# Kernel optimization log

Hardware: AMD Instinct MI355X
Metric: run time of the kernel (lower is better)

Reference implementation:

```python
import jax, jax.numpy as jnp
import numpy as np

N = 100000
NNZ = 3200000
F = 128


def setup_inputs() -> dict:
    key = jax.random.key(0)
    k1, k2, k3 = jax.random.split(key, 3)
    x = jax.random.normal(k1, (N, F), dtype=jnp.float32)
    A_ind = jax.random.randint(k2, (2, NNZ), 0, N, dtype=jnp.int64)
    A_val = jax.random.normal(k3, (NNZ,), dtype=jnp.float32)
    return {"x": x, "A_ind": A_ind, "A_val": A_val}


def reference(x, A_ind, A_val):
    # COO SpMM: out[r] = sum over edges e with row[e]==r of A_val[e] * x[col[e]]
    # coalesce() in torch sums duplicate (row, col) entries; segment_sum over
    # rows yields identical math without explicit sorting/deduplication.
    row, col = A_ind[0], A_ind[1]
    contrib = A_val[:, None] * x[col]            # [nnz, F] gather + scale
    out = jax.ops.segment_sum(contrib, row, num_segments=x.shape[0])  # scatter-add
    return out
```

## Files before the change

### kernel.cpp

```cpp
#include <hip/hip_runtime.h>

#define F 128
#define RPB 64
#define MAXNB 1792
#define CHUNK 8192
#define EPT 32
#define CAP 3072
#define SPMM_T 512
#define HELD (CAP/SPMM_T)
#define PERSIST 1024

__global__ void spmm_coo_atomic(const int* __restrict__ rows,
                                const int* __restrict__ cols,
                                const float* __restrict__ vals,
                                const float* __restrict__ x,
                                float* __restrict__ out,
                                int nnz, int n_rows) {
    int t = blockIdx.x * blockDim.x + threadIdx.x;
    int e = t >> 5;
    int g = t & 31;
    if (e >= nnz) return;
    int r = rows[e];
    int c = cols[e];
    float v = vals[e];
    if ((unsigned)r >= (unsigned)n_rows || (unsigned)c >= (unsigned)n_rows) return;
    const float4 xv = *reinterpret_cast<const float4*>(x + (size_t)c * F + g * 4);
    float* o = out + (size_t)r * F + g * 4;
    atomicAdd(o + 0, v * xv.x);
    atomicAdd(o + 1, v * xv.y);
    atomicAdd(o + 2, v * xv.z);
    atomicAdd(o + 3, v * xv.w);
}

__device__ __forceinline__ unsigned f2bf(float f) {
    unsigned u = __float_as_uint(f);
    return (u + 0x7FFFu + ((u >> 16) & 1u)) >> 16;
}

__global__ void k_cvt_histo(const float* __restrict__ x, unsigned short* __restrict__ xb,
                            long long xtotal,
                            const int* __restrict__ rows, int* __restrict__ cnt,
                            int nnz, int nbk, int n, int cvtb) {
    __shared__ int lc[MAXNB];
    if ((int)blockIdx.x < cvtb) {
        long long i = ((long long)blockIdx.x * 256 + threadIdx.x) * 8;
        if (i >= xtotal) return;
        float4 a = *reinterpret_cast<const float4*>(x + i);
        float4 b = *reinterpret_cast<const float4*>(x + i + 4);
        uint4 o;
        o.x = f2bf(a.x) | (f2bf(a.y) << 16);
        o.y = f2bf(a.z) | (f2bf(a.w) << 16);
        o.z = f2bf(b.x) | (f2bf(b.y) << 16);
        o.w = f2bf(b.z) | (f2bf(b.w) << 16);
        *reinterpret_cast<uint4*>(xb + i) = o;
    } else {
        for (int i = threadIdx.x; i < nbk; i += 256) lc[i] = 0;
        __syncthreads();
        int base = ((int)blockIdx.x - cvtb) * CHUNK;
#pragma unroll
        for (int k = 0; k < EPT; ++k) {
            int e = base + k * 256 + threadIdx.x;
            if (e < nnz) {
                int r = rows[e];
                if ((unsigned)r < (unsigned)n) atomicAdd(&lc[r / RPB], 1);
            }
        }
        __syncthreads();
        for (int i = threadIdx.x; i < nbk; i += 256) {
            int c = lc[i];
            if (c) atomicAdd(&cnt[i], c);
        }
    }
}

__global__ void k_bucket_scan(const int* __restrict__ cnt, int* __restrict__ off,
                              int* __restrict__ gcur, int nbk) {
    __shared__ int s[256];
    int tid = threadIdx.x;
    int per = (nbk + 255) / 256;
    int base = tid * per;
    int loc[8];
    int tsum = 0;
#pragma unroll
    for (int k = 0; k < 8; ++k) {
        int i = base + k;
        int v = (k < per && i < nbk) ? cnt[i] : 0;
        loc[k] = v;
        tsum += v;
    }
    s[tid] = tsum;
    __syncthreads();
    for (int o = 1; o < 256; o <<= 1) {
        int t = (tid >= o) ? s[tid - o] : 0;
        __syncthreads();
        s[tid] += t;
        __syncthreads();
    }
    int run = s[tid] - tsum;
#pragma unroll
    for (int k = 0; k < 8; ++k) {
        int i = base + k;
        if (k < per && i < nbk) { off[i] = run; gcur[i] = run; }
        run += loc[k];
    }
    if (tid == 255) off[nbk] = s[255];
}

__global__ void k_rank_scatter(const int* __restrict__ rows, const int* __restrict__ cols,
                               const float* __restrict__ vals, int* __restrict__ gcur,
                               int2* __restrict__ pair, int nnz, int nbk, int n) {
    __shared__ int lcnt[MAXNB];
    __shared__ int lbase[MAXNB];
    for (int i = threadIdx.x; i < nbk; i += 256) lcnt[i] = 0;
    __syncthreads();
    int base = blockIdx.x * CHUNK;
    unsigned br[EPT];
#pragma unroll
    for (int k = 0; k < EPT; ++k) {
        int e = base + k * 256 + threadIdx.x;
        br[k] = 0xFFFFFFFFu;
        if (e < nnz) {
            int r = rows[e];
            if ((unsigned)r < (unsigned)n) {
                int b = r / RPB;
                int rk = atomicAdd(&lcnt[b], 1);
                br[k] = ((unsigned)b << 13) | (unsigned)rk;
            }
        }
    }
    __syncthreads();
    for (int i = threadIdx.x; i < nbk; i += 256) {
        int c = lcnt[i];
        if (c) lbase[i] = atomicAdd(&gcur[i], c);
    }
    __syncthreads();
#pragma unroll
    for (int k = 0; k < EPT; ++k) {
        if (br[k] != 0xFFFFFFFFu) {
            int e = base + k * 256 + threadIdx.x;
            int b = br[k] >> 13;
            int rk = br[k] & 0x1FFF;
            int lr = rows[e] - b * RPB;
            int c = cols[e];
            if ((unsigned)c >= (unsigned)n) c = 0;
            int pos = lbase[b] + rk;
            pair[pos] = make_int2((lr << 17) | c, __float_as_int(vals[e]));
        }
    }
}

__global__ void __launch_bounds__(SPMM_T) k_sort_spmm(const int* __restrict__ off,
                                                      const int2* __restrict__ pair,
                                                      const unsigned short* __restrict__ xb,
                                                      float* __restrict__ out,
                                                      int n, int nbk) {
    __shared__ int2 eb[CAP];
    __shared__ int rcnt[RPB];
    __shared__ int rst[RPB + 1];
    __shared__ int rcur[RPB];

    int tid = threadIdx.x;
    int wave = tid >> 6;
    int lane = tid & 63;
    int q = lane >> 4;
    int fl = lane & 15;

    for (int b = blockIdx.x; b < nbk; b += gridDim.x) {
        int beg = off[b], end = off[b + 1];
        bool first = true;
        int bb = beg;
        do {
            int bn = min(CAP, end - bb);
            if (tid < RPB) rcnt[tid] = 0;
            __syncthreads();

            int2 held[HELD];
#pragma unroll
            for (int k = 0; k < HELD; ++k) {
                int j = tid + k * SPMM_T;
                held[k] = make_int2(0, 0);
                if (j < bn) {
                    int2 pr = pair[bb + j];
                    held[k] = pr;
                    atomicAdd(&rcnt[pr.x >> 17], 1);
                }
            }
            __syncthreads();

            if (tid < RPB) {
                int v = rcnt[tid];
                int s = v;
                for (int o = 1; o < RPB; o <<= 1) {
                    int t = __shfl_up(s, o);
                    if (tid >= o) s += t;
                }
                rst[tid + 1] = s;
                if (tid == 0) rst[0] = 0;
                rcur[tid] = s - v;
            }
            __syncthreads();

#pragma unroll
            for (int k = 0; k < HELD; ++k) {
                int j = tid + k * SPMM_T;
                if (j < bn) {
                    int2 pr = held[k];
                    int lr = pr.x >> 17;
                    int pos = atomicAdd(&rcur[lr], 1);
                    eb[pos] = make_int2(pr.x & 0x1FFFF, pr.y);
                }
            }
            __syncthreads();

            for (int rr = 0; rr < 8; ++rr) {
                int lr = wave * 8 + rr;
                int s0 = rst[lr], s1 = rst[lr + 1];
                float acc[8] = {0.f, 0.f, 0.f, 0.f, 0.f, 0.f, 0.f, 0.f};
#pragma unroll 2
                for (int j = s0 + q; j < s1; j += 4) {
                    int2 e = eb[j];
                    int col = e.x;
                    float vk = __int_as_float(e.y);
                    uint4 w = *reinterpret_cast<const uint4*>(xb + (size_t)col * F + fl * 8);
                    acc[0] += vk * __uint_as_float(w.x << 16);
                    acc[1] += vk * __uint_as_float(w.x & 0xFFFF0000u);
                    acc[2] += vk * __uint_as_float(w.y << 16);
                    acc[3] += vk * __uint_as_float(w.y & 0xFFFF0000u);
                    acc[4] += vk * __uint_as_float(w.z << 16);
                    acc[5] += vk * __uint_as_float(w.z & 0xFFFF0000u);
                    acc[6] += vk * __uint_as_float(w.w << 16);
                    acc[7] += vk * __uint_as_float(w.w & 0xFFFF0000u);
                }
#pragma unroll
                for (int i = 0; i < 8; ++i) {
                    acc[i] += __shfl_xor(acc[i], 16);
                    acc[i] += __shfl_xor(acc[i], 32);
                }
                if (q == 0) {
                    long long row = (long long)b * RPB + lr;
                    if (row < n) {
                        float* po = out + (size_t)row * F + fl * 8;
                        float4 lo = make_float4(acc[0], acc[1], acc[2], acc[3]);
                        float4 hi = make_float4(acc[4], acc[5], acc[6], acc[7]);
                        if (first) {
                            *reinterpret_cast<float4*>(po) = lo;
                            *reinterpret_cast<float4*>(po + 4) = hi;
                        } else {
                            float4 t0 = *reinterpret_cast<const float4*>(po);
                            float4 t1 = *reinterpret_cast<const float4*>(po + 4);
                            t0.x += lo.x; t0.y += lo.y; t0.z += lo.z; t0.w += lo.w;
                            t1.x += hi.x; t1.y += hi.y; t1.z += hi.z; t1.w += hi.w;
                            *reinterpret_cast<float4*>(po) = t0;
                            *reinterpret_cast<float4*>(po + 4) = t1;
                        }
                    }
                }
            }
            first = false;
            bb += CAP;
            __syncthreads();
        } while (bb < end);
    }
}

extern "C" void kernel_launch(void* const* d_in, const int* in_sizes, int n_in,
                              void* d_out, int out_size, void* d_ws, size_t ws_size,
                              hipStream_t stream) {
    const float* x = (const float*)d_in[0];
    const int* A_ind = (const int*)d_in[1];
    const float* A_val = (const float*)d_in[2];
    float* out = (float*)d_out;

    const int nnz = in_sizes[2];
    const int n = out_size / F;
    const int nbk = (n + RPB - 1) / RPB;
    const int* rows = A_ind;
    const int* cols = A_ind + nnz;

    const long long xtotal = (long long)n * F;

    const size_t need = (size_t)nnz * 8
                      + (size_t)xtotal * 2
                      + (size_t)(3 * nbk + 1) * 4 + 128;

    if (nbk > MAXNB || (xtotal % 8) != 0 || ws_size < need) {
        hipMemsetAsync(d_out, 0, (size_t)out_size * sizeof(float), stream);
        const long long total = (long long)nnz * 32;
        spmm_coo_atomic<<<(int)((total + 255) / 256), 256, 0, stream>>>(
            rows, cols, A_val, x, out, nnz, n);
        return;
    }

    char* w = (char*)d_ws;
    int2* pair = (int2*)w;            w += (size_t)nnz * 8;
    unsigned short* xb = (unsigned short*)w;  w += (size_t)xtotal * 2;
    int* cnt = (int*)w;               w += (size_t)nbk * 4;
    int* off = (int*)w;               w += (size_t)(nbk + 1) * 4;
    int* gcur = (int*)w;

    const int nchunks = (nnz + CHUNK - 1) / CHUNK;
    const int cvtb = (int)((xtotal / 8 + 255) / 256);

    hipMemsetAsync(cnt, 0, (size_t)nbk * 4, stream);
    k_cvt_histo<<<cvtb + nchunks, 256, 0, stream>>>(x, xb, xtotal, rows, cnt,
                                                    nnz, nbk, n, cvtb);
    k_bucket_scan<<<1, 256, 0, stream>>>(cnt, off, gcur, nbk);
    k_rank_scatter<<<nchunks, 256, 0, stream>>>(rows, cols, A_val, gcur, pair,
                                                nnz, nbk, n);
    const int pgrid = (nbk < PERSIST) ? nbk : PERSIST;
    k_sort_spmm<<<pgrid, SPMM_T, 0, stream>>>(off, pair, xb, out, n, nbk);
}
```

Baseline: 216.7 us.

## Split bucket sort and SpMM into row-sort kernel and fine-grained per-row SpMM

New measurement: 238.7 us. 10.2% more time.

```diff
diff --git a/kernel.cpp b/kernel.cpp
--- a/kernel.cpp
+++ b/kernel.cpp
@@ -5,10 +5,9 @@
 #define MAXNB 1792
 #define CHUNK 8192
 #define EPT 32
-#define CAP 3072
-#define SPMM_T 512
-#define HELD (CAP/SPMM_T)
-#define PERSIST 1024
+#define CAPR 3072
+#define HELDR (CAPR/256)
+#define SPMM_T 256
 
 __global__ void spmm_coo_atomic(const int* __restrict__ rows,
                                 const int* __restrict__ cols,
@@ -74,9 +73,10 @@
 }
 
 __global__ void k_bucket_scan(const int* __restrict__ cnt, int* __restrict__ off,
-                              int* __restrict__ gcur, int nbk) {
+                              int* __restrict__ gcur, int* __restrict__ bflag, int nbk) {
     __shared__ int s[256];
     int tid = threadIdx.x;
+    for (int i = tid; i < nbk; i += 256) bflag[i] = 0;
     int per = (nbk + 255) / 256;
     int base = tid * per;
     int loc[8];
@@ -149,78 +149,118 @@
     }
 }
 
-__global__ void __launch_bounds__(SPMM_T) k_sort_spmm(const int* __restrict__ off,
-                                                      const int2* __restrict__ pair,
-                                                      const unsigned short* __restrict__ xb,
-                                                      float* __restrict__ out,
-                                                      int n, int nbk) {
-    __shared__ int2 eb[CAP];
-    __shared__ int rcnt[RPB];
-    __shared__ int rst[RPB + 1];
-    __shared__ int rcur[RPB];
-
+__global__ void __launch_bounds__(256) k_rowsort(const int* __restrict__ off,
+                                                 int2* __restrict__ pair,
+                                                 int* __restrict__ rowoff,
+                                                 int* __restrict__ bflag,
+                                                 int nbk, int n) {
+    __shared__ int cnt[RPB];
+    __shared__ int cur[RPB];
+    int b = blockIdx.x;
+    int tid = threadIdx.x;
+    int beg = off[b], end = off[b + 1];
+    int bn = end - beg;
+    if (b == 0 && tid == 0) rowoff[n] = off[nbk];
+
+    if (bn > CAPR) {
+        if (tid == 0) bflag[b] = 1;
+        for (int r = tid; r < RPB; r += 256) {
+            int idx = b * RPB + r;
+            if (idx <= n) rowoff[idx] = beg;
+        }
+        return;
+    }
+    if (tid < RPB) cnt[tid] = 0;
+    __syncthreads();
+
+    int2 held[HELDR];
+#pragma unroll
+    for (int k = 0; k < HELDR; ++k) {
+        int j = tid + k * 256;
+        held[k] = make_int2(-1, 0);
+        if (j < bn) {
+            held[k] = pair[beg + j];
+            atomicAdd(&cnt[held[k].x >> 17], 1);
+        }
+    }
+    __syncthreads();
+    if (tid < RPB) {
+        int v = cnt[tid];
+        int s = v;
+        for (int o = 1; o < RPB; o <<= 1) {
+            int t = __shfl_up(s, o);
+            if (tid >= o) s += t;
+        }
+        int start = beg + s - v;
+        cur[tid] = start;
+        int idx = b * RPB + tid;
+        if (idx <= n) rowoff[idx] = start;
+    }
+    __syncthreads();
+#pragma unroll
+    for (int k = 0; k < HELDR; ++k) {
+        if (held[k].x != -1) {
+            int lr = held[k].x >> 17;
+            int pos = atomicAdd(&cur[lr], 1);
+            pair[pos] = make_int2(held[k].x & 0x1FFFF, held[k].y);
+        }
+    }
+}
+
+__global__ void __launch_bounds__(SPMM_T) k_spmm8(const int* __restrict__ rowoff,
+                                                  const int2* __restrict__ pair,
+                                                  const int* __restrict__ off,
+                                                  const int* __restrict__ bflag,
+                                                  const unsigned short* __restrict__ xb,
+                                                  float* __restrict__ out, int n) {
     int tid = threadIdx.x;
     int wave = tid >> 6;
     int lane = tid & 63;
     int q = lane >> 4;
     int fl = lane & 15;
-
-    for (int b = blockIdx.x; b < nbk; b += gridDim.x) {
-        int beg = off[b], end = off[b + 1];
-        bool first = true;
-        int bb = beg;
-        do {
-            int bn = min(CAP, end - bb);
-            if (tid < RPB) rcnt[tid] = 0;
-            __syncthreads();
-
-            int2 held[HELD];
-#pragma unroll
-            for (int k = 0; k < HELD; ++k) {
-                int j = tid + k * SPMM_T;
-                held[k] = make_int2(0, 0);
-                if (j < bn) {
-                    int2 pr = pair[bb + j];
-                    held[k] = pr;
-                    atomicAdd(&rcnt[pr.x >> 17], 1);
+    int rbase = blockIdx.x * 8;
+    int b = rbase / RPB;
+    bool slow = (bflag[b] != 0);
+
+    for (int rr = 0; rr < 2; ++rr) {
+        int row = rbase + wave * 2 + rr;
+        if (row < n) {
+            float acc[8] = {0.f, 0.f, 0.f, 0.f, 0.f, 0.f, 0.f, 0.f};
+            if (!slow) {
+                int s0 = rowoff[row], s1 = rowoff[row + 1];
+                for (int jb = s0; jb < s1; jb += 16) {
+#pragma unroll
+                    for (int k = 0; k < 4; ++k) {
+                        int j = jb + q + k * 4;
+                        int col = 0;
+                        float vk = 0.f;
+                        if (j < s1) {
+                            int2 e = pair[j];
+                            col = e.x;
+                            vk = __int_as_float(e.y);
+                        }
+                        uint4 w = *reinterpret_cast<const uint4*>(xb + (size_t)col * F + fl * 8);
+                        acc[0] += vk * __uint_as_float(w.x << 16);
+                        acc[1] += vk * __uint_as_float(w.x & 0xFFFF0000u);
+                        acc[2] += vk * __uint_as_float(w.y << 16);
+                        acc[3] += vk * __uint_as_float(w.y & 0xFFFF0000u);
+                        acc[4] += vk * __uint_as_float(w.z << 16);
+                        acc[5] += vk * __uint_as_float(w.z & 0xFFFF0000u);
+                        acc[6] += vk * __uint_as_float(w.w << 16);
+                        acc[7] += vk * __uint_as_float(w.w & 0xFFFF0000u);
+                    }
                 }
-            }
-            __syncthreads();
-
-            if (tid < RPB) {
-                int v = rcnt[tid];
-                int s = v;
-                for (int o = 1; o < RPB; o <<= 1) {
-                    int t = __shfl_up(s, o);
-                    if (tid >= o) s += t;
-                }
-                rst[tid + 1] = s;
-                if (tid == 0) rst[0] = 0;
-                rcur[tid] = s - v;
-            }
-            __syncthreads();
-
-#pragma unroll
-            for (int k = 0; k < HELD; ++k) {
-                int j = tid + k * SPMM_T;
-                if (j < bn) {
-                    int2 pr = held[k];
-                    int lr = pr.x >> 17;
-                    int pos = atomicAdd(&rcur[lr], 1);
-                    eb[pos] = make_int2(pr.x & 0x1FFFF, pr.y);
-                }
-            }
-            __syncthreads();
-
-            for (int rr = 0; rr < 8; ++rr) {
-                int lr = wave * 8 + rr;
-                int s0 = rst[lr], s1 = rst[lr + 1];
-                float acc[8] = {0.f, 0.f, 0.f, 0.f, 0.f, 0.f, 0.f, 0.f};
-#pragma unroll 2
-                for (int j = s0 + q; j < s1; j += 4) {
-                    int2 e = eb[j];
-                    int col = e.x;
-                    float vk = __int_as_float(e.y);
+            } else {
+                int beg = off[b], end = off[b + 1];
+                int lrw = row - b * RPB;
+                for (int j = beg + q; j < end; j += 4) {
+                    int2 e = pair[j];
+                    int col = 0;
+                    float vk = 0.f;
+                    if ((e.x >> 17) == lrw) {
+                        col = e.x & 0x1FFFF;
+                        vk = __int_as_float(e.y);
+                    }
                     uint4 w = *reinterpret_cast<const uint4*>(xb + (size_t)col * F + fl * 8);
                     acc[0] += vk * __uint_as_float(w.x << 16);
                     acc[1] += vk * __uint_as_float(w.x & 0xFFFF0000u);
@@ -231,35 +271,18 @@
                     acc[6] += vk * __uint_as_float(w.w << 16);
                     acc[7] += vk * __uint_as_float(w.w & 0xFFFF0000u);
                 }
-#pragma unroll
-                for (int i = 0; i < 8; ++i) {
-                    acc[i] += __shfl_xor(acc[i], 16);
-                    acc[i] += __shfl_xor(acc[i], 32);
-                }
-                if (q == 0) {
-                    long long row = (long long)b * RPB + lr;
-                    if (row < n) {
-                        float* po = out + (size_t)row * F + fl * 8;
-                        float4 lo = make_float4(acc[0], acc[1], acc[2], acc[3]);
-                        float4 hi = make_float4(acc[4], acc[5], acc[6], acc[7]);
-                        if (first) {
-                            *reinterpret_cast<float4*>(po) = lo;
-                            *reinterpret_cast<float4*>(po + 4) = hi;
-                        } else {
-                            float4 t0 = *reinterpret_cast<const float4*>(po);
-                            float4 t1 = *reinterpret_cast<const float4*>(po + 4);
-                            t0.x += lo.x; t0.y += lo.y; t0.z += lo.z; t0.w += lo.w;
-                            t1.x += hi.x; t1.y += hi.y; t1.z += hi.z; t1.w += hi.w;
-                            *reinterpret_cast<float4*>(po) = t0;
-                            *reinterpret_cast<float4*>(po + 4) = t1;
-                        }
-                    }
-                }
-            }
-            first = false;
-            bb += CAP;
-            __syncthreads();
-        } while (bb < end);
+            }
+#pragma unroll
+            for (int i = 0; i < 8; ++i) {
+                acc[i] += __shfl_xor(acc[i], 16);
+                acc[i] += __shfl_xor(acc[i], 32);
+            }
+            if (q == 0) {
+                float* po = out + (size_t)row * F + fl * 8;
+                *reinterpret_cast<float4*>(po) = make_float4(acc[0], acc[1], acc[2], acc[3]);
+                *reinterpret_cast<float4*>(po + 4) = make_float4(acc[4], acc[5], acc[6], acc[7]);
+            }
+        }
     }
 }
 
@@ -281,7 +304,8 @@
 
     const size_t need = (size_t)nnz * 8
                       + (size_t)xtotal * 2
-                      + (size_t)(3 * nbk + 1) * 4 + 128;
+                      + (size_t)(n + RPB + 1) * 4
+                      + (size_t)(4 * nbk + 1) * 4 + 256;
 
     if (nbk > MAXNB || (xtotal % 8) != 0 || ws_size < need) {
         hipMemsetAsync(d_out, 0, (size_t)out_size * sizeof(float), stream);
@@ -294,9 +318,11 @@
     char* w = (char*)d_ws;
     int2* pair = (int2*)w;            w += (size_t)nnz * 8;
     unsigned short* xb = (unsigned short*)w;  w += (size_t)xtotal * 2;
+    int* rowoff = (int*)w;            w += (size_t)(n + RPB + 1) * 4;
     int* cnt = (int*)w;               w += (size_t)nbk * 4;
     int* off = (int*)w;               w += (size_t)(nbk + 1) * 4;
-    int* gcur = (int*)w;
+    int* gcur = (int*)w;              w += (size_t)nbk * 4;
+    int* bflag = (int*)w;
 
     const int nchunks = (nnz + CHUNK - 1) / CHUNK;
     const int cvtb = (int)((xtotal / 8 + 255) / 256);
@@ -304,9 +330,10 @@
     hipMemsetAsync(cnt, 0, (size_t)nbk * 4, stream);
     k_cvt_histo<<<cvtb + nchunks, 256, 0, stream>>>(x, xb, xtotal, rows, cnt,
                                                     nnz, nbk, n, cvtb);
-    k_bucket_scan<<<1, 256, 0, stream>>>(cnt, off, gcur, nbk);
+    k_bucket_scan<<<1, 256, 0, stream>>>(cnt, off, gcur, bflag, nbk);
     k_rank_scatter<<<nchunks, 256, 0, stream>>>(rows, cols, A_val, gcur, pair,
                                                 nnz, nbk, n);
-    const int pgrid = (nbk < PERSIST) ? nbk : PERSIST;
-    k_sort_spmm<<<pgrid, SPMM_T, 0, stream>>>(off, pair, xb, out, n, nbk);
-}
+    k_rowsort<<<nbk, 256, 0, stream>>>(off, pair, rowoff, bflag, nbk, n);
+    const int sgrid = (n + 7) / 8;
+    k_spmm8<<<sgrid, SPMM_T, 0, stream>>>(rowoff, pair, off, bflag, xb, out, n);
+}
```

## Stage bucket scatter in shared memory for contiguous global writes

Applied to the files above, without the earlier changes.

Result: slower. 282.2 us (+30.2%).

```diff
diff --git a/kernel.cpp b/kernel.cpp
--- a/kernel.cpp
+++ b/kernel.cpp
@@ -9,6 +9,9 @@
 #define SPMM_T 512
 #define HELD (CAP/SPMM_T)
 #define PERSIST 1024
+#define SCHUNK 7168
+#define SEPT 14
+#define MAXNB2 1600
 
 __global__ void spmm_coo_atomic(const int* __restrict__ rows,
                                 const int* __restrict__ cols,
@@ -106,46 +109,98 @@
     if (tid == 255) off[nbk] = s[255];
 }
 
-__global__ void k_rank_scatter(const int* __restrict__ rows, const int* __restrict__ cols,
-                               const float* __restrict__ vals, int* __restrict__ gcur,
-                               int2* __restrict__ pair, int nnz, int nbk, int n) {
-    __shared__ int lcnt[MAXNB];
-    __shared__ int lbase[MAXNB];
-    for (int i = threadIdx.x; i < nbk; i += 256) lcnt[i] = 0;
-    __syncthreads();
-    int base = blockIdx.x * CHUNK;
-    unsigned br[EPT];
-#pragma unroll
-    for (int k = 0; k < EPT; ++k) {
-        int e = base + k * 256 + threadIdx.x;
-        br[k] = 0xFFFFFFFFu;
+__global__ void __launch_bounds__(512) k_stage_scatter(
+        const int* __restrict__ rows, const int* __restrict__ cols,
+        const float* __restrict__ vals, int* __restrict__ gcur,
+        int2* __restrict__ pair, int nnz, int nbk, int n) {
+    __shared__ int2 eb[SCHUNK];
+    __shared__ int lcnt[MAXNB2];
+    __shared__ int lcur[MAXNB2];
+    __shared__ int lbase[MAXNB2];
+    __shared__ int s[512];
+    int tid = threadIdx.x;
+    for (int i = tid; i < nbk; i += 512) lcnt[i] = 0;
+    __syncthreads();
+
+    int base = blockIdx.x * SCHUNK;
+    int heldp[SEPT];
+    int heldv[SEPT];
+    short heldb[SEPT];
+#pragma unroll
+    for (int k = 0; k < SEPT; ++k) {
+        int e = base + k * 512 + tid;
+        heldb[k] = -1;
+        heldp[k] = 0;
+        heldv[k] = 0;
         if (e < nnz) {
             int r = rows[e];
             if ((unsigned)r < (unsigned)n) {
                 int b = r / RPB;
-                int rk = atomicAdd(&lcnt[b], 1);
-                br[k] = ((unsigned)b << 13) | (unsigned)rk;
-            }
-        }
-    }
-    __syncthreads();
-    for (int i = threadIdx.x; i < nbk; i += 256) {
+                int lr = r - b * RPB;
+                int c = cols[e];
+                if ((unsigned)c >= (unsigned)n) c = 0;
+                heldp[k] = (lr << 17) | c;
+                heldv[k] = __float_as_int(vals[e]);
+                heldb[k] = (short)b;
+                atomicAdd(&lcnt[b], 1);
+            }
+        }
+    }
+    __syncthreads();
+
+    {
+        int per = (nbk + 511) / 512;
+        int sbase = tid * per;
+        int loc[4];
+        int tsum = 0;
+#pragma unroll
+        for (int k = 0; k < 4; ++k) {
+            int i = sbase + k;
+            int v = (k < per && i < nbk) ? lcnt[i] : 0;
+            loc[k] = v; tsum += v;
+        }
+        s[tid] = tsum;
+        __syncthreads();
+        for (int o = 1; o < 512; o <<= 1) {
+            int t = (tid >= o) ? s[tid - o] : 0;
+            __syncthreads();
+            s[tid] += t;
+            __syncthreads();
+        }
+        int run = s[tid] - tsum;
+#pragma unroll
+        for (int k = 0; k < 4; ++k) {
+            int i = sbase + k;
+            if (k < per && i < nbk) lcur[i] = run;
+            run += loc[k];
+        }
+    }
+    __syncthreads();
+
+    for (int i = tid; i < nbk; i += 512) {
         int c = lcnt[i];
         if (c) lbase[i] = atomicAdd(&gcur[i], c);
     }
     __syncthreads();
-#pragma unroll
-    for (int k = 0; k < EPT; ++k) {
-        if (br[k] != 0xFFFFFFFFu) {
-            int e = base + k * 256 + threadIdx.x;
-            int b = br[k] >> 13;
-            int rk = br[k] & 0x1FFF;
-            int lr = rows[e] - b * RPB;
-            int c = cols[e];
-            if ((unsigned)c >= (unsigned)n) c = 0;
-            int pos = lbase[b] + rk;
-            pair[pos] = make_int2((lr << 17) | c, __float_as_int(vals[e]));
-        }
+
+#pragma unroll
+    for (int k = 0; k < SEPT; ++k) {
+        if (heldb[k] >= 0) {
+            int pos = atomicAdd(&lcur[(int)heldb[k]], 1);
+            eb[pos] = make_int2(heldp[k], heldv[k]);
+        }
+    }
+    __syncthreads();
+
+    int gid = tid >> 3, glane = tid & 7;
+    for (int bi = gid; bi < nbk; bi += 64) {
+        int len = lcnt[bi];
+        if (len == 0) continue;
+        int end = lcur[bi];
+        int start = end - len;
+        int gb = lbase[bi];
+        for (int j = glane; j < len; j += 8)
+            pair[gb + j] = eb[start + j];
     }
 }
 
@@ -189,14 +244,14 @@
 
             if (tid < RPB) {
                 int v = rcnt[tid];
-                int s = v;
+                int sc = v;
                 for (int o = 1; o < RPB; o <<= 1) {
-                    int t = __shfl_up(s, o);
-                    if (tid >= o) s += t;
-                }
-                rst[tid + 1] = s;
+                    int t = __shfl_up(sc, o);
+                    if (tid >= o) sc += t;
+                }
+                rst[tid + 1] = sc;
                 if (tid == 0) rst[0] = 0;
-                rcur[tid] = s - v;
+                rcur[tid] = sc - v;
             }
             __syncthreads();
 
@@ -283,7 +338,7 @@
                       + (size_t)xtotal * 2
                       + (size_t)(3 * nbk + 1) * 4 + 128;
 
-    if (nbk > MAXNB || (xtotal % 8) != 0 || ws_size < need) {
+    if (nbk > MAXNB2 || (xtotal % 8) != 0 || ws_size < need) {
         hipMemsetAsync(d_out, 0, (size_t)out_size * sizeof(float), stream);
         const long long total = (long long)nnz * 32;
         spmm_coo_atomic<<<(int)((total + 255) / 256), 256, 0, stream>>>(
@@ -300,13 +355,14 @@
 
     const int nchunks = (nnz + CHUNK - 1) / CHUNK;
     const int cvtb = (int)((xtotal / 8 + 255) / 256);
+    const int nsc = (nnz + SCHUNK - 1) / SCHUNK;
 
     hipMemsetAsync(cnt, 0, (size_t)nbk * 4, stream);
     k_cvt_histo<<<cvtb + nchunks, 256, 0, stream>>>(x, xb, xtotal, rows, cnt,
                                                     nnz, nbk, n, cvtb);
     k_bucket_scan<<<1, 256, 0, stream>>>(cnt, off, gcur, nbk);
-    k_rank_scatter<<<nchunks, 256, 0, stream>>>(rows, cols, A_val, gcur, pair,
-                                                nnz, nbk, n);
+    k_stage_scatter<<<nsc, 512, 0, stream>>>(rows, cols, A_val, gcur, pair,
+                                             nnz, nbk, n);
     const int pgrid = (nbk < PERSIST) ? nbk : PERSIST;
     k_sort_spmm<<<pgrid, SPMM_T, 0, stream>>>(off, pair, xb, out, n, nbk);
 }
```
